# Performance work log

Measured on AMD Instinct MI355X. Metric: run time of the kernel, lower is better.

Reference implementation:

```python
import jax, jax.numpy as jnp
import numpy as np

F = 16  # ConvLSTM2D filters

def hard_sigmoid(x):
    # Keras (TF2) hard_sigmoid: clip(0.2*x + 0.5, 0, 1) -- ConvLSTM2D default recurrent_activation
    return jnp.clip(0.2 * x + 0.5, 0.0, 1.0)

def convlstm_1x1(x, W, U, b, reverse):
    # x: [B,T,H,W,C]; W: [C,4F]; U: [F,4F]; b: [4F]
    # 1x1 ConvLSTM2D == per-pixel LSTM; gate order in Keras kernel: i, f, c, o
    B, T, H, Wd, C = x.shape
    xs = jnp.moveaxis(x, 1, 0)  # [T,B,H,W,C]
    h0 = jnp.zeros((B, H, Wd, F), x.dtype)
    c0 = jnp.zeros((B, H, Wd, F), x.dtype)
    def step(carry, xt):
        h, c = carry
        z = jnp.einsum('bhwc,cf->bhwf', xt, W) + jnp.einsum('bhwc,cf->bhwf', h, U) + b
        i, f, g, o = jnp.split(z, 4, axis=-1)
        i = hard_sigmoid(i); f = hard_sigmoid(f); o = hard_sigmoid(o)
        c_new = f * c + i * jnp.tanh(g)
        h_new = o * jnp.tanh(c_new)
        return (h_new, c_new), h_new
    # reverse=True: scan runs backward in time, ys aligned to input order,
    # which matches Keras Bidirectional(go_backwards + output re-reversal).
    _, hs = jax.lax.scan(step, (h0, c0), xs, reverse=reverse)
    return jnp.moveaxis(hs, 0, 1)  # [B,T,H,W,F]

def setup_inputs() -> dict:
    key = jax.random.key(0)
    ks = jax.random.split(key, 13)
    B, T, H, Wd, C = 16, 64, 32, 32, 32
    s = 0.1
    inp = {
        'inputs': jax.random.normal(ks[0], (B, T, H, Wd, C), jnp.float32),
        'Wf': jax.random.normal(ks[1], (C, 4 * F), jnp.float32) * s,
        'Uf': jax.random.normal(ks[2], (F, 4 * F), jnp.float32) * s,
        'bf': jnp.zeros((4 * F,), jnp.float32),
        'Wb': jax.random.normal(ks[3], (C, 4 * F), jnp.float32) * s,
        'Ub': jax.random.normal(ks[4], (F, 4 * F), jnp.float32) * s,
        'bb': jnp.zeros((4 * F,), jnp.float32),
        'w1': jax.random.normal(ks[5], (2 * F, 16), jnp.float32) * s,
        'b1': jnp.zeros((16,), jnp.float32),
        'w2': jax.random.normal(ks[6], (16, 16), jnp.float32) * s,
        'b2': jnp.zeros((16,), jnp.float32),
        'w3': jax.random.normal(ks[7], (16, 10), jnp.float32) * s,
        'b3': jnp.zeros((10,), jnp.float32),
    }
    return inp

def reference(inputs, Wf, Uf, bf, Wb, Ub, bb, w1, b1, w2, b2, w3, b3):
    h_fwd = convlstm_1x1(inputs, Wf, Uf, bf, reverse=False)
    h_bwd = convlstm_1x1(inputs, Wb, Ub, bb, reverse=True)
    x = jnp.concatenate([h_fwd, h_bwd], axis=-1)  # [B,T,H,W,2F]
    x = jnp.einsum('...c,cd->...d', x, w1) + b1
    x = jnp.einsum('...c,cd->...d', x, w2) + b2
    x = jnp.einsum('...c,cd->...d', x, w3) + b3
    return x  # [B,T,H,W,10]
```

## Files before the change

kernel.cpp:

```cpp
#include <hip/hip_runtime.h>
#include <hip/hip_bf16.h>
#include <cstdint>
#include <cstddef>

#define TT 64
#define CC 32
#define FF 16
#define HWSZ 1024
#define NPIX 16384

typedef __attribute__((ext_vector_type(8))) short  short8;
typedef __attribute__((ext_vector_type(4))) short  short4v;
typedef __attribute__((ext_vector_type(4))) float  f32x4;

__device__ __forceinline__ float bf2f(unsigned int u16) {
  union { unsigned int u; float f; } c;
  c.u = u16 << 16;
  return c.f;
}
__device__ __forceinline__ unsigned int f2bf(float f) {
  union { float f; unsigned int u; } c;
  c.f = f;
  unsigned int u = c.u;
  return (u + 0x7fffu + ((u >> 16) & 1u)) >> 16;
}
__device__ __forceinline__ unsigned int pkbf(float a, float b) {
  float2 f2; f2.x = a; f2.y = b;
  __hip_bfloat162 h = __float22bfloat162_rn(f2);
  union { __hip_bfloat162 h; unsigned int u; } c; c.h = h;
  return c.u;
}
__device__ __forceinline__ float clamp01(float x) {
  return fminf(fmaxf(x, 0.0f), 1.0f);
}

#define L2E2 2.8853900817779268f
__device__ __forceinline__ float tanh_e2(float e2arg) {
  const float e = __builtin_exp2f(e2arg);
  const float t = __builtin_amdgcn_rcpf(e + 1.0f);
  return fmaf(-2.0f, t, 1.0f);
}

__global__ __launch_bounds__(512) void fold_kernel(
    const float* __restrict__ w1, const float* __restrict__ b1,
    const float* __restrict__ w2, const float* __restrict__ b2,
    const float* __restrict__ w3, const float* __restrict__ b3,
    float* __restrict__ Wc, float* __restrict__ bc)
{
  __shared__ float w23[16 * 10];
  __shared__ float bb2[16];
  const int t = threadIdx.x;

  if (t < 160) {
    const int k = t / 10, j = t % 10;
    float s = 0.0f;
    #pragma unroll
    for (int m = 0; m < 16; ++m) s = fmaf(w2[k * 16 + m], w3[m * 10 + j], s);
    w23[t] = s;
  }
  if (t < 16) {
    float s = b2[t];
    #pragma unroll
    for (int m = 0; m < 16; ++m) s = fmaf(b1[m], w2[m * 16 + t], s);
    bb2[t] = s;
  }
  __syncthreads();
  if (t < 320) {
    const int k = t / 10, j = t % 10;
    float s = 0.0f;
    #pragma unroll
    for (int m = 0; m < 16; ++m) s = fmaf(w1[k * 16 + m], w23[m * 10 + j], s);
    Wc[t] = s;
  }
  if (t < 10) {
    float s = b3[t];
    #pragma unroll
    for (int m = 0; m < 16; ++m) s = fmaf(bb2[m], w3[m * 10 + t], s);
    bc[t] = s;
  }
}

__global__ __launch_bounds__(256, 2) void lstm_kernel(
    const float* __restrict__ x,
    const float* __restrict__ Wf, const float* __restrict__ Uf, const float* __restrict__ bfp,
    const float* __restrict__ Wb, const float* __restrict__ Ub, const float* __restrict__ bbp,
    unsigned short* __restrict__ hf_out, unsigned short* __restrict__ hb_out)
{
  const int dir = blockIdx.y;
  const float* __restrict__ Wp = dir ? Wb : Wf;
  const float* __restrict__ Up = dir ? Ub : Uf;
  const float* __restrict__ bp = dir ? bbp : bfp;
  unsigned short* __restrict__ hout = dir ? hb_out : hf_out;

  const int tid  = threadIdx.x;
  const int lane = tid & 63;
  const int wid  = tid >> 6;
  const int quad = lane >> 4;
  const int l15  = lane & 15;

  const int px  = (blockIdx.x * 4 + wid) * 16 + l15;
  const int b   = px >> 10;
  const int hwi = px & 1023;

  short8  AW[4];
  short4v AU[4];
  #pragma unroll
  for (int nt = 0; nt < 4; ++nt) {
    short8 vw;
    #pragma unroll
    for (int j = 0; j < 8; ++j) {
      const int k   = quad * 8 + j;
      const int col = nt * 16 + l15;
      vw[j] = (short)f2bf(Wp[k * 64 + col]);
    }
    AW[nt] = vw;
    short4v vu;
    #pragma unroll
    for (int j = 0; j < 4; ++j) {
      const int k   = quad * 4 + j;
      const int col = nt * 16 + l15;
      vu[j] = (short)f2bf(Up[k * 64 + col]);
    }
    AU[nt] = vu;
  }

  float bi[4], bfv[4], bgl[4], bo[4];
  #pragma unroll
  for (int r = 0; r < 4; ++r) {
    const int f = quad * 4 + r;
    bi[r]  = fmaf(bp[ 0 + f], 0.2f, 0.5f);
    bfv[r] = fmaf(bp[16 + f], 0.2f, 0.5f);
    bgl[r] = bp[32 + f] * L2E2;
    bo[r]  = fmaf(bp[48 + f], 0.2f, 0.5f);
  }

  float cst[4] = {0.f, 0.f, 0.f, 0.f};
  union BU  { short8  s8; int i[4]; };
  union BH  { short4v s4; int i[2]; };
  BH Bh; Bh.i[0] = 0; Bh.i[1] = 0;

  const int t0 = dir ? (TT - 1) : 0;
  const unsigned int pos0 = (unsigned int)((b * TT + t0) * HWSZ + hwi);
  const int xstep = dir ? -(HWSZ * CC * 4) : (HWSZ * CC * 4);
  const int hstep = dir ? -(HWSZ * 32) : (HWSZ * 32);
  unsigned int hob = pos0 * 32 + quad * 8;

  const char* xb = (const char*)x;
  char* hbb = (char*)hout;

  const unsigned int xo0 = pos0 * (CC * 4) + quad * 32;
  float4 t0a = *reinterpret_cast<const float4*>(xb + xo0);
  float4 t0b = *reinterpret_cast<const float4*>(xb + xo0 + 16);
  unsigned int xoff = xo0 + xstep;
  float4 b1a = *reinterpret_cast<const float4*>(xb + xoff);
  float4 b1b = *reinterpret_cast<const float4*>(xb + xoff + 16);
  xoff += xstep;
  float4 b2a = *reinterpret_cast<const float4*>(xb + xoff);
  float4 b2b = *reinterpret_cast<const float4*>(xb + xoff + 16);
  xoff += xstep;
  float4 b3a = *reinterpret_cast<const float4*>(xb + xoff);
  float4 b3b = *reinterpret_cast<const float4*>(xb + xoff + 16);
  xoff += xstep;
  float4 b0a = *reinterpret_cast<const float4*>(xb + xoff);
  float4 b0b = *reinterpret_cast<const float4*>(xb + xoff + 16);

  f32x4 zx[4];
  {
    BU ax;
    ax.i[0] = pkbf(t0a.x, t0a.y); ax.i[1] = pkbf(t0a.z, t0a.w);
    ax.i[2] = pkbf(t0b.x, t0b.y); ax.i[3] = pkbf(t0b.z, t0b.w);
    const f32x4 zz = {0.f, 0.f, 0.f, 0.f};
    #pragma unroll
    for (int nt = 0; nt < 4; ++nt)
      zx[nt] = __builtin_amdgcn_mfma_f32_16x16x32_bf16(AW[nt], ax.s8, zz, 0, 0, 0);
  }

#define STEP(S, BA, BB) do {                                                   \
            \
    f32x4 z_[4];                                                               \
    _Pragma("unroll")                                                          \
    for (int nt = 0; nt < 4; ++nt)                                             \
      z_[nt] = __builtin_amdgcn_mfma_f32_16x16x16bf16_1k(AU[nt], Bh.s4, zx[nt], 0, 0, 0); \
                     \
    {                                                                          \
      BU ax;                                                                   \
      ax.i[0] = pkbf(BA.x, BA.y); ax.i[1] = pkbf(BA.z, BA.w);                  \
      ax.i[2] = pkbf(BB.x, BB.y); ax.i[3] = pkbf(BB.z, BB.w);                  \
      const f32x4 zzv = {0.f, 0.f, 0.f, 0.f};                                  \
      _Pragma("unroll")                                                        \
      for (int nt = 0; nt < 4; ++nt)                                           \
        zx[nt] = __builtin_amdgcn_mfma_f32_16x16x32_bf16(AW[nt], ax.s8, zzv, 0, 0, 0); \
    }                                                                          \
          \
    if ((S) + 5 < TT) xoff += xstep;                                           \
    BA = *reinterpret_cast<const float4*>(xb + xoff);                          \
    BB = *reinterpret_cast<const float4*>(xb + xoff + 16);                     \
                              \
    float hv[4];                                                               \
    _Pragma("unroll")                                                          \
    for (int r = 0; r < 4; ++r) {                                              \
      const float ig = clamp01(fmaf(z_[0][r], 0.2f, bi[r]));                   \
      const float fg = clamp01(fmaf(z_[1][r], 0.2f, bfv[r]));                  \
      const float og = clamp01(fmaf(z_[3][r], 0.2f, bo[r]));                   \
      const float gg = tanh_e2(fmaf(z_[2][r], L2E2, bgl[r]));                  \
      cst[r] = fmaf(fg, cst[r], ig * gg);                                      \
      hv[r]  = og * tanh_e2(cst[r] * L2E2);                                    \
    }                                                                          \
            \
    Bh.i[0] = (int)pkbf(hv[0], hv[1]);                       \
    Bh.i[1] = (int)pkbf(hv[2], hv[3]);                     \
         \
    *reinterpret_cast<int2*>(hbb + hob) = make_int2(Bh.i[0], Bh.i[1]);         \
    hob += hstep;                                                              \
  } while (0)

  for (int sb = 0; sb < TT; sb += 4) {
    STEP(sb + 0, b1a, b1b);
    STEP(sb + 1, b2a, b2b);
    STEP(sb + 2, b3a, b3b);
    STEP(sb + 3, b0a, b0b);
  }
#undef STEP
}

__global__ __launch_bounds__(256) void dense_kernel(
    const unsigned short* __restrict__ hf, const unsigned short* __restrict__ hb,
    const float* __restrict__ Wc, const float* __restrict__ bc,
    float* __restrict__ out)
{
  const int tid  = threadIdx.x;
  const int lane = tid & 63;
  const int quad = lane >> 4;
  const int l15  = lane & 15;

  short8 Bhi, Blo;
  #pragma unroll
  for (int j = 0; j < 8; ++j) {
    const int k = quad * 8 + j;
    const float v  = (l15 < 10) ? Wc[k * 10 + l15] : 0.0f;
    const unsigned int hi = f2bf(v);
    const float lo = v - bf2f(hi);
    Bhi[j] = (short)hi;
    Blo[j] = (short)f2bf(lo);
  }
  const float bcv = (l15 < 10) ? bc[l15] : 0.0f;

  const unsigned short* __restrict__ src = (quad & 2) ? hb : hf;
  const unsigned int lsub = (quad & 1) * 8;

  const unsigned int gw = (blockIdx.x * 256 + tid) >> 6;

  #pragma unroll
  for (int i = 0; i < 8; ++i) {
    const unsigned int tile  = gw * 8 + i;
    const unsigned int pos16 = tile * 16 + l15;
    const short8 A = *reinterpret_cast<const short8*>(src + pos16 * 16 + lsub);

    f32x4 acc = {bcv, bcv, bcv, bcv};
    acc = __builtin_amdgcn_mfma_f32_16x16x32_bf16(A, Bhi, acc, 0, 0, 0);
    acc = __builtin_amdgcn_mfma_f32_16x16x32_bf16(A, Blo, acc, 0, 0, 0);

    if (l15 < 10) {
      const unsigned int rowbase = tile * 16 + quad * 4;
      #pragma unroll
      for (int r = 0; r < 4; ++r) {
        out[(size_t)(rowbase + r) * 10 + l15] = acc[r];
      }
    }
  }
}

extern "C" void kernel_launch(void* const* d_in, const int* in_sizes, int n_in,
                              void* d_out, int out_size, void* d_ws, size_t ws_size,
                              hipStream_t stream) {
  const float* x   = (const float*)d_in[0];
  const float* Wf  = (const float*)d_in[1];
  const float* Uf  = (const float*)d_in[2];
  const float* bfp = (const float*)d_in[3];
  const float* Wb  = (const float*)d_in[4];
  const float* Ub  = (const float*)d_in[5];
  const float* bbp = (const float*)d_in[6];
  const float* w1  = (const float*)d_in[7];
  const float* b1  = (const float*)d_in[8];
  const float* w2  = (const float*)d_in[9];
  const float* b2  = (const float*)d_in[10];
  const float* w3  = (const float*)d_in[11];
  const float* b3  = (const float*)d_in[12];

  unsigned short* hfbuf = (unsigned short*)d_ws;
  unsigned short* hbbuf = hfbuf + (size_t)NPIX * TT * FF;
  float* Wc = (float*)(hbbuf + (size_t)NPIX * TT * FF);
  float* bc = Wc + 320;

  fold_kernel<<<1, 512, 0, stream>>>(w1, b1, w2, b2, w3, b3, Wc, bc);

  lstm_kernel<<<dim3(256, 2), 256, 0, stream>>>(x, Wf, Uf, bfp, Wb, Ub, bbp, hfbuf, hbbuf);

  dense_kernel<<<2048, 256, 0, stream>>>(hfbuf, hbbuf, Wc, bc, (float*)d_out);
}
```

Before: 270.8 us.

## Fuse folded dense head into LSTM kernel via atomic output accumulation

The separate dense kernel and the bf16 hidden-state round trip through workspace are removed. Each direction's LSTM step now multiplies its hidden state by its half of the folded dense weights with two MFMAs (hi/lo split) and atomically adds the result into the output, which is zeroed first by a memset. This removes writing and re-reading about 64 MB of hidden states and one launch. In exchange it adds float atomics to 10-float output rows, whose summation order is nondeterministic, plus a scheduling barrier in the step.

```diff
diff --git a/kernel.cpp b/kernel.cpp
--- a/kernel.cpp
+++ b/kernel.cpp
@@ -39,6 +39,10 @@
   const float e = __builtin_exp2f(e2arg);
   const float t = __builtin_amdgcn_rcpf(e + 1.0f);
   return fmaf(-2.0f, t, 1.0f);
+}
+
+__device__ __forceinline__ void gatomic_fadd(float* p, float v) {
+  unsafeAtomicAdd(p, v);
 }
 
 __global__ __launch_bounds__(512) void fold_kernel(
@@ -84,13 +88,13 @@
     const float* __restrict__ x,
     const float* __restrict__ Wf, const float* __restrict__ Uf, const float* __restrict__ bfp,
     const float* __restrict__ Wb, const float* __restrict__ Ub, const float* __restrict__ bbp,
-    unsigned short* __restrict__ hf_out, unsigned short* __restrict__ hb_out)
+    const float* __restrict__ Wc, const float* __restrict__ bc,
+    float* __restrict__ out)
 {
   const int dir = blockIdx.y;
   const float* __restrict__ Wp = dir ? Wb : Wf;
   const float* __restrict__ Up = dir ? Ub : Uf;
   const float* __restrict__ bp = dir ? bbp : bfp;
-  unsigned short* __restrict__ hout = dir ? hb_out : hf_out;
 
   const int tid  = threadIdx.x;
   const int lane = tid & 63;
@@ -124,6 +128,24 @@
     AU[nt] = vu;
   }
 
+  const int kbase = dir ? 16 : 0;
+  short4v DWhi, DWlo;
+  #pragma unroll
+  for (int j = 0; j < 4; ++j) {
+    const int k = kbase + quad * 4 + j;
+    const float v = (l15 < 10) ? Wc[k * 10 + l15] : 0.0f;
+    const unsigned int hi = f2bf(v);
+    const float lo = v - bf2f(hi);
+    DWhi[j] = (short)hi;
+    DWlo[j] = (short)f2bf(lo);
+  }
+  float bcv[4];
+  #pragma unroll
+  for (int r = 0; r < 4; ++r) {
+    const int m = quad * 4 + r;
+    bcv[r] = (dir == 0 && m < 10) ? bc[m] : 0.0f;
+  }
+
   float bi[4], bfv[4], bgl[4], bo[4];
   #pragma unroll
   for (int r = 0; r < 4; ++r) {
@@ -142,11 +164,10 @@
   const int t0 = dir ? (TT - 1) : 0;
   const unsigned int pos0 = (unsigned int)((b * TT + t0) * HWSZ + hwi);
   const int xstep = dir ? -(HWSZ * CC * 4) : (HWSZ * CC * 4);
-  const int hstep = dir ? -(HWSZ * 32) : (HWSZ * 32);
-  unsigned int hob = pos0 * 32 + quad * 8;
+  const int ostep = dir ? -(HWSZ * 10) : (HWSZ * 10);
+  unsigned int oidx = pos0 * 10 + quad * 4;
 
   const char* xb = (const char*)x;
-  char* hbb = (char*)hout;
 
   const unsigned int xo0 = pos0 * (CC * 4) + quad * 32;
   float4 t0a = *reinterpret_cast<const float4*>(xb + xo0);
@@ -195,6 +216,8 @@
     if ((S) + 5 < TT) xoff += xstep;                                           \
     BA = *reinterpret_cast<const float4*>(xb + xoff);                          \
     BB = *reinterpret_cast<const float4*>(xb + xoff + 16);                     \
+                \
+    __builtin_amdgcn_sched_barrier(0x0F);                                      \
                               \
     float hv[4];                                                               \
     _Pragma("unroll")                                                          \
@@ -209,9 +232,17 @@
             \
     Bh.i[0] = (int)pkbf(hv[0], hv[1]);                       \
     Bh.i[1] = (int)pkbf(hv[2], hv[3]);                     \
-         \
-    *reinterpret_cast<int2*>(hbb + hob) = make_int2(Bh.i[0], Bh.i[1]);         \
-    hob += hstep;                                                              \
+      \
+    {                                                                          \
+      f32x4 acc = {bcv[0], bcv[1], bcv[2], bcv[3]};                            \
+      acc = __builtin_amdgcn_mfma_f32_16x16x16bf16_1k(DWhi, Bh.s4, acc, 0, 0, 0); \
+      acc = __builtin_amdgcn_mfma_f32_16x16x16bf16_1k(DWlo, Bh.s4, acc, 0, 0, 0); \
+      _Pragma("unroll")                                                        \
+      for (int r = 0; r < 4; ++r) {                                            \
+        if (quad * 4 + r < 10) gatomic_fadd(out + oidx + r, acc[r]);           \
+      }                                                                        \
+    }                                                                          \
+    oidx += ostep;                                                             \
   } while (0)
 
   for (int sb = 0; sb < TT; sb += 4) {
@@ -221,53 +252,6 @@
     STEP(sb + 3, b0a, b0b);
   }
 #undef STEP
-}
-
-__global__ __launch_bounds__(256) void dense_kernel(
-    const unsigned short* __restrict__ hf, const unsigned short* __restrict__ hb,
-    const float* __restrict__ Wc, const float* __restrict__ bc,
-    float* __restrict__ out)
-{
-  const int tid  = threadIdx.x;
-  const int lane = tid & 63;
-  const int quad = lane >> 4;
-  const int l15  = lane & 15;
-
-  short8 Bhi, Blo;
-  #pragma unroll
-  for (int j = 0; j < 8; ++j) {
-    const int k = quad * 8 + j;
-    const float v  = (l15 < 10) ? Wc[k * 10 + l15] : 0.0f;
-    const unsigned int hi = f2bf(v);
-    const float lo = v - bf2f(hi);
-    Bhi[j] = (short)hi;
-    Blo[j] = (short)f2bf(lo);
-  }
-  const float bcv = (l15 < 10) ? bc[l15] : 0.0f;
-
-  const unsigned short* __restrict__ src = (quad & 2) ? hb : hf;
-  const unsigned int lsub = (quad & 1) * 8;
-
-  const unsigned int gw = (blockIdx.x * 256 + tid) >> 6;
-
-  #pragma unroll
-  for (int i = 0; i < 8; ++i) {
-    const unsigned int tile  = gw * 8 + i;
-    const unsigned int pos16 = tile * 16 + l15;
-    const short8 A = *reinterpret_cast<const short8*>(src + pos16 * 16 + lsub);
-
-    f32x4 acc = {bcv, bcv, bcv, bcv};
-    acc = __builtin_amdgcn_mfma_f32_16x16x32_bf16(A, Bhi, acc, 0, 0, 0);
-    acc = __builtin_amdgcn_mfma_f32_16x16x32_bf16(A, Blo, acc, 0, 0, 0);
-
-    if (l15 < 10) {
-      const unsigned int rowbase = tile * 16 + quad * 4;
-      #pragma unroll
-      for (int r = 0; r < 4; ++r) {
-        out[(size_t)(rowbase + r) * 10 + l15] = acc[r];
-      }
-    }
-  }
 }
 
 extern "C" void kernel_launch(void* const* d_in, const int* in_sizes, int n_in,
@@ -287,14 +271,13 @@
   const float* w3  = (const float*)d_in[11];
   const float* b3  = (const float*)d_in[12];
 
-  unsigned short* hfbuf = (unsigned short*)d_ws;
-  unsigned short* hbbuf = hfbuf + (size_t)NPIX * TT * FF;
-  float* Wc = (float*)(hbbuf + (size_t)NPIX * TT * FF);
+  float* Wc = (float*)d_ws;
   float* bc = Wc + 320;
 
+  hipMemsetAsync(d_out, 0, (size_t)out_size, stream);
+
   fold_kernel<<<1, 512, 0, stream>>>(w1, b1, w2, b2, w3, b3, Wc, bc);
 
-  lstm_kernel<<<dim3(256, 2), 256, 0, stream>>>(x, Wf, Uf, bfp, Wb, Ub, bbp, hfbuf, hbbuf);
-
-  dense_kernel<<<2048, 256, 0, stream>>>(hfbuf, hbbuf, Wc, bc, (float*)d_out);
-}
+  lstm_kernel<<<dim3(256, 2), 256, 0, stream>>>(x, Wf, Uf, bfp, Wb, Ub, bbp,
+                                                Wc, bc, (float*)d_out);
+}
```

Result: slower. 444.6 us (+64.2%).
